# Performance work log

Measured on AMD Instinct MI355X. Metric: run time of the kernel, lower is better.

The kernel has to match this reference:

```python
import math
import jax, jax.numpy as jnp
import numpy as np

B, N, NR, DA, E, H, NB = 2, 2048, 256, 256, 768, 12, 2
DH = E // H
NQ, NK = 32, 128
INF = 1e10


def _layernorm(x, g=None, b=None, eps=1e-5):
    mu = x.mean(-1, keepdims=True)
    var = ((x - mu) ** 2).mean(-1, keepdims=True)
    y = (x - mu) * jax.lax.rsqrt(var + eps)
    if g is not None:
        y = y * g + b
    return y


def _fourier(x):
    # NeRF-style: freqs = 2**linspace(0,12,64); out dim = 3*(1+2*64) = 387
    freqs = 2.0 ** jnp.linspace(0.0, 12.0, 64)
    ang = (x[..., None, :] * freqs[:, None]).reshape(*x.shape[:-1], -1)  # (...,192)
    return jnp.concatenate([x, jnp.sin(ang), jnp.cos(ang)], -1)


def _abs_pos(pos):
    # sinusoidal absolute PE, embed_dim=DA//2, include_input -> DA//2 + 1 dims
    d = DA // 2
    div = jnp.exp(jnp.arange(0, d, 2, dtype=jnp.float32) * (-math.log(10000.0) / d))
    ang = pos * div  # (B,N,1)*(d/2,) -> (B,N,d/2)
    return jnp.concatenate([pos, jnp.sin(ang), jnp.cos(ang)], -1)


def _local_bias(n, nq, nk):
    # vectorized create_local_attn_bias: block-diagonal local window mask
    i = jnp.arange(n)
    blk = i // nq
    lo = jnp.maximum(0, nq * blk - (nk - nq) // 2)
    hi = nq * blk + (nq + nk) // 2
    j = jnp.arange(n)
    allowed = (j[None, :] >= lo[:, None]) & (j[None, :] < hi[:, None])
    return jnp.where(allowed, 0.0, -INF).astype(jnp.float32)


def _rope(x, pos):
    # x: (B,H,N,DH), pos: (B,N) float
    half = DH // 2
    inv = 1.0 / (10000.0 ** (jnp.arange(half, dtype=jnp.float32) / half))
    ang = pos[:, None, :, None] * inv  # (B,1,N,half)
    c, s = jnp.cos(ang), jnp.sin(ang)
    x1, x2 = x[..., :half], x[..., half:]
    return jnp.concatenate([x1 * c - x2 * s, x1 * s + x2 * c], -1)


def setup_inputs() -> dict:
    key = jax.random.key(0)
    def rn(i, shape, s=1.0):
        return jax.random.normal(jax.random.fold_in(key, i), shape, jnp.float32) * s
    LF = 387 + (DA // 2 + 1) + 408  # 924
    tok = (jnp.arange(N) * NR) // N  # each atom's residue index (sorted)
    inp = {
        'atom_coords': rn(0, (B, N, 3), 10.0),
        'ref_pos': rn(1, (B, N, 3), 10.0),
        'res_id': jnp.broadcast_to(tok[None, :, None], (B, N, 1)).astype(jnp.int32),
        'res_type_feat': rn(2, (B, N, 23)),
        'charge': rn(3, (B, N, 1)),
        'atomic_number': rn(4, (B, N, 128)),
        'atom_name_feat': rn(5, (B, N, 256)),
        'adaLN_emb': rn(6, (B, DA)),
        'rope_pos': jnp.broadcast_to(jnp.arange(N, dtype=jnp.int32)[None], (B, N)),
        'atom_to_token': jnp.broadcast_to(jax.nn.one_hot(tok, NR, dtype=jnp.float32)[None], (B, N, NR)),
        'feat_W': rn(7, (LF, DA), 0.02), 'feat_b': jnp.zeros(DA), 'feat_ln_g': jnp.ones(DA), 'feat_ln_b': jnp.zeros(DA),
        'pos_W': rn(8, (387, DA), 0.02),
        'in_W': rn(9, (2 * DA, DA), 0.02),
        'tin_W': rn(10, (DA, E), 0.02), 'tin_b': jnp.zeros(E), 'tin_ln_g': jnp.ones(E), 'tin_ln_b': jnp.zeros(E),
        'ada_W': rn(11, (DA, E), 0.02), 'ada_b': jnp.zeros(E), 'ada_ln_g': jnp.ones(E), 'ada_ln_b': jnp.zeros(E),
        'blk_mod_W': rn(12, (NB, E, 6 * E), 0.02), 'blk_mod_b': jnp.zeros((NB, 6 * E)),
        'blk_qkv_W': rn(13, (NB, E, 3 * E), 0.02), 'blk_qkv_b': jnp.zeros((NB, 3 * E)),
        'blk_o_W': rn(14, (NB, E, E), 0.02), 'blk_o_b': jnp.zeros((NB, E)),
        'blk_m1_W': rn(15, (NB, E, 4 * E), 0.02), 'blk_m1_b': jnp.zeros((NB, 4 * E)),
        'blk_m2_W': rn(16, (NB, 4 * E, E), 0.02), 'blk_m2_b': jnp.zeros((NB, E)),
        'tout_W': rn(17, (E, DA), 0.02), 'tout_b': jnp.zeros(DA), 'tout_ln_g': jnp.ones(DA), 'tout_ln_b': jnp.zeros(DA),
    }
    return inp


def reference(atom_coords, ref_pos, res_id, res_type_feat, charge, atomic_number,
              atom_name_feat, adaLN_emb, rope_pos, atom_to_token,
              feat_W, feat_b, feat_ln_g, feat_ln_b, pos_W, in_W,
              tin_W, tin_b, tin_ln_g, tin_ln_b, ada_W, ada_b, ada_ln_g, ada_ln_b,
              blk_mod_W, blk_mod_b, blk_qkv_W, blk_qkv_b, blk_o_W, blk_o_b,
              blk_m1_W, blk_m1_b, blk_m2_W, blk_m2_b,
              tout_W, tout_b, tout_ln_g, tout_ln_b):
    # feature fusion
    ref_pos_emb = _fourier(ref_pos)                                   # (B,N,387)
    atom_res_pos = _abs_pos(res_id.astype(jnp.float32))               # (B,N,129)
    feats = jnp.concatenate([ref_pos_emb, res_type_feat, atom_res_pos,
                             charge, atomic_number, atom_name_feat], -1)  # (B,N,924)
    feats = jax.nn.silu(_layernorm(feats @ feat_W + feat_b, feat_ln_g, feat_ln_b))
    coords = _fourier(atom_coords) @ pos_W                            # (B,N,DA)
    atom_in = jnp.concatenate([feats, coords], -1) @ in_W             # (B,N,DA)
    x = _layernorm(atom_in @ tin_W + tin_b, tin_ln_g, tin_ln_b)       # (B,N,E)
    c = _layernorm(adaLN_emb @ ada_W + ada_b, ada_ln_g, ada_ln_b)     # (B,E)

    bias = _local_bias(N, NQ, NK)                                     # (N,N)
    pos = rope_pos.astype(jnp.float32)
    scale = 1.0 / math.sqrt(DH)
    for l in range(NB):  # small fixed layer count
        m = jax.nn.silu(c) @ blk_mod_W[l] + blk_mod_b[l]
        sh1, sc1, g1, sh2, sc2, g2 = jnp.split(m, 6, -1)              # each (B,E)
        h = _layernorm(x) * (1 + sc1[:, None]) + sh1[:, None]
        qkv = (h @ blk_qkv_W[l] + blk_qkv_b[l]).reshape(B, N, 3, H, DH)
        q, k, v = [qkv[:, :, i].transpose(0, 2, 1, 3) for i in range(3)]  # (B,H,N,DH)
        q, k = _rope(q, pos), _rope(k, pos)
        scores = jnp.einsum('bhqd,bhkd->bhqk', q, k) * scale + bias
        attn = jax.nn.softmax(scores, -1)
        o = jnp.einsum('bhqk,bhkd->bhqd', attn, v).transpose(0, 2, 1, 3).reshape(B, N, E)
        x = x + g1[:, None] * (o @ blk_o_W[l] + blk_o_b[l])
        h2 = _layernorm(x) * (1 + sc2[:, None]) + sh2[:, None]
        x = x + g2[:, None] * (jax.nn.gelu(h2 @ blk_m1_W[l] + blk_m1_b[l]) @ blk_m2_W[l] + blk_m2_b[l])

    atom_latent = _layernorm(x @ tout_W + tout_b, tout_ln_g, tout_ln_b)   # (B,N,DA)
    a2t = atom_to_token / (atom_to_token.sum(1, keepdims=True) + 1e-6)    # segment-mean weights
    residue_latent = jnp.einsum('bnr,bnd->brd', a2t, atom_latent)         # (B,NR,DA)
    return residue_latent, atom_latent
```

## Files before the change

### kernel.cpp

```cpp
#include <hip/hip_runtime.h>
#include <hip/hip_bf16.h>
#include <math.h>

#define B_ 2
#define N_ 2048
#define NR_ 256
#define DA_ 256
#define E_ 768
#define H_ 12
#define DH_ 64
#define NB_ 2

typedef __attribute__((ext_vector_type(8))) __bf16 bf16x8;
typedef __attribute__((ext_vector_type(4))) float f32x4;

union U8 { bf16x8 v; __hip_bfloat16 e[8]; unsigned short u[8]; };
union U4 { __hip_bfloat16 e[4]; uint2 u2; };

__device__ __forceinline__ void gload16(const void* g, void* l) {
    __builtin_amdgcn_global_load_lds(
        (const __attribute__((address_space(1))) void*)g,
        (__attribute__((address_space(3))) void*)l, 16, 0, 0);
}

__device__ __forceinline__ float bsum256(float v, float* red4, int tid) {
    #pragma unroll
    for (int m = 32; m > 0; m >>= 1) v += __shfl_xor(v, m, 64);
    __syncthreads();
    if ((tid & 63) == 0) red4[tid >> 6] = v;
    __syncthreads();
    return red4[0] + red4[1] + red4[2] + red4[3];
}

__global__ __launch_bounds__(128) void build_feats_kernel(
    const float* __restrict__ atom_coords, const float* __restrict__ ref_pos,
    const int* __restrict__ res_id, const float* __restrict__ res_type,
    const float* __restrict__ charge, const float* __restrict__ atomic_number,
    const float* __restrict__ atom_name, const int* __restrict__ rope_pos,
    __hip_bfloat16* __restrict__ feats, __hip_bfloat16* __restrict__ coordsF,
    float* __restrict__ ropeC, float* __restrict__ ropeS)
{
    int a = blockIdx.x;
    int tid = threadIdx.x;
    __hip_bfloat16* f  = feats   + (size_t)a * 1024;
    __hip_bfloat16* cf = coordsF + (size_t)a * 512;

    float rp[3], cc[3];
    #pragma unroll
    for (int i = 0; i < 3; ++i) { rp[i] = ref_pos[(size_t)a*3 + i]; cc[i] = atom_coords[(size_t)a*3 + i]; }

    if (tid < 3) { f[tid] = __float2bfloat16(rp[tid]); cf[tid] = __float2bfloat16(cc[tid]); }

    if (tid >= 64 && tid < 96) {
        int dd = tid - 64;
        float rpos = (float)rope_pos[a];
        float ang = rpos * expf(-0.28782313662425574f * (float)dd);
        float sn, cs; sincosf(ang, &sn, &cs);
        ropeC[a*32 + dd] = cs; ropeS[a*32 + dd] = sn;
    }

    for (int s = tid; s < 192; s += 128) {
        int fi = s / 3, ci = s % 3;
        float freq = exp2f(12.f * (float)fi / 63.f);
        float ar = rp[ci] * freq;
        float ac = cc[ci] * freq;
        float snr, csr, snc, csc_;
        sincosf(ar, &snr, &csr);
        sincosf(ac, &snc, &csc_);
        f[3 + s]    = __float2bfloat16(snr);  f[195 + s]  = __float2bfloat16(csr);
        cf[3 + s]   = __float2bfloat16(snc);  cf[195 + s] = __float2bfloat16(csc_);
    }
    if (tid < 23) f[387 + tid] = __float2bfloat16(res_type[(size_t)a*23 + tid]);

    float pos = (float)res_id[a];
    if (tid == 0) f[410] = __float2bfloat16(pos);
    if (tid < 64) {
        float div = expf(-9.210340371976184f / 128.f * (float)(2 * tid));
        float ang = pos * div;
        float sn, cs; sincosf(ang, &sn, &cs);
        f[411 + tid] = __float2bfloat16(sn);
        f[475 + tid] = __float2bfloat16(cs);
    }
    if (tid == 0) f[539] = __float2bfloat16(charge[a]);
    if (tid < 128) f[540 + tid] = __float2bfloat16(atomic_number[(size_t)a*128 + tid]);
    for (int s = tid; s < 256; s += 128) f[668 + s] = __float2bfloat16(atom_name[(size_t)a*256 + s]);
    if (tid < 100) f[924 + tid] = __float2bfloat16(0.f);
    if (tid < 125) cf[387 + tid] = __float2bfloat16(0.f);
}

__global__ __launch_bounds__(256) void transconv_kernel(
    const float* __restrict__ W, __hip_bfloat16* __restrict__ WT,
    int Ksrc, int Kdst, int Nn, size_t wstride, size_t tstride)
{
    __shared__ float t[32][33];
    W  += (size_t)blockIdx.z * wstride;
    WT += (size_t)blockIdx.z * tstride;
    int n0 = blockIdx.x * 32, k0 = blockIdx.y * 32;
    int tid = threadIdx.x;
    int tx = tid & 31, ty = tid >> 5;
    #pragma unroll
    for (int i = 0; i < 4; ++i) {
        int k = k0 + ty + i*8;
        t[ty + i*8][tx] = (k < Ksrc) ? W[(size_t)k * Nn + n0 + tx] : 0.f;
    }
    __syncthreads();
    #pragma unroll
    for (int i = 0; i < 4; ++i) {
        int row = ty + i*8;
        WT[(size_t)(n0 + row) * Kdst + k0 + tx] = __float2bfloat16(t[tx][row]);
    }
}

__device__ __forceinline__ float epi_apply(float v, int grow, int gcol,
    const float* bias, int mode, const float* X, int ldx,
    const float* gate, int gstride)
{
    if (bias) v += bias[gcol];
    if (mode == 1) {
        float u = 1.5957691216057308f * (v + 0.044715f * v * v * v);
        v = v / (1.f + __expf(-u));
    } else if (mode == 2) {
        int b = grow >> 11;
        v = X[(size_t)grow * ldx + gcol] + gate[(size_t)b * gstride + gcol] * v;
    } else if (mode == 3) {
        v = v * gate[grow];
    }
    return v;
}

__global__ __launch_bounds__(256) void gemm_bf16_kernel(
    const __hip_bfloat16* __restrict__ A, int lda,
    const __hip_bfloat16* __restrict__ BT, int ldb,
    const float* __restrict__ bias,
    void* __restrict__ C, int ldc,
    int K, int mode, int obf,
    const float* __restrict__ X, int ldx,
    const float* __restrict__ gate, int gstride,
    float* __restrict__ P,
    int mtiles, size_t bstrideA, size_t bstrideB)
{
    __shared__ __hip_bfloat16 As[3][128 * 32];
    __shared__ __hip_bfloat16 Bs[3][128 * 32];

    int gx = gridDim.x;
    int nwg = gx * gridDim.y;
    int fo = blockIdx.y * gx + blockIdx.x;
    int ft = (fo & 7) * (nwg >> 3) + (fo >> 3);
    int bx = ft % gx, by = ft / gx;

    int bb  = by / mtiles;
    int m0l = (by % mtiles) * 128;
    int m0g = by * 128;
    int n0 = bx * 128;
    const __hip_bfloat16* Ab  = A  + (size_t)bb * bstrideA;
    const __hip_bfloat16* BTb = BT + (size_t)bb * bstrideB;
    int nz = gridDim.z;
    int Kh = K / nz;
    int kb = blockIdx.z * Kh;
    int nIter = Kh >> 5;
    int tid = threadIdx.x;
    int w = tid >> 6, l = tid & 63;
    int wr = (w >> 1) * 64, wc = (w & 1) * 64;
    int lr = l & 15, lg = l >> 4;
    int slot = ((lg ^ ((lr >> 1) & 3)) & 3) * 8;

    int seg0 = tid,        row0s = seg0 >> 2, g0 = (seg0 & 3) ^ ((row0s >> 1) & 3);
    int seg1 = 256 + tid,  row1s = seg1 >> 2, g1 = (seg1 & 3) ^ ((row1s >> 1) & 3);

    f32x4 acc[4][4];
    #pragma unroll
    for (int i = 0; i < 4; ++i)
        #pragma unroll
        for (int j = 0; j < 4; ++j)
            acc[i][j] = f32x4{0.f, 0.f, 0.f, 0.f};

    {
        gload16(Ab  + (size_t)(m0l + row0s) * lda + kb + g0 * 8, (char*)As[0] + seg0 * 16);
        gload16(BTb + (size_t)(n0 + row0s) * ldb + kb + g0 * 8, (char*)Bs[0] + seg0 * 16);
        gload16(Ab  + (size_t)(m0l + row1s) * lda + kb + g1 * 8, (char*)As[0] + seg1 * 16);
        gload16(BTb + (size_t)(n0 + row1s) * ldb + kb + g1 * 8, (char*)Bs[0] + seg1 * 16);
        if (nIter > 1) {
            int k1 = kb + 32;
            gload16(Ab  + (size_t)(m0l + row0s) * lda + k1 + g0 * 8, (char*)As[1] + seg0 * 16);
            gload16(BTb + (size_t)(n0 + row0s) * ldb + k1 + g0 * 8, (char*)Bs[1] + seg0 * 16);
            gload16(Ab  + (size_t)(m0l + row1s) * lda + k1 + g1 * 8, (char*)As[1] + seg1 * 16);
            gload16(BTb + (size_t)(n0 + row1s) * ldb + k1 + g1 * 8, (char*)Bs[1] + seg1 * 16);
        }
    }

    int cur = 0;
    for (int it = 0; it < nIter; ++it) {
        if (it + 1 < nIter) asm volatile("s_waitcnt vmcnt(4)" ::: "memory");
        else                asm volatile("s_waitcnt vmcnt(0)" ::: "memory");
        __builtin_amdgcn_s_barrier();
        __builtin_amdgcn_sched_barrier(0);
        if (it + 2 < nIter) {
            int nb = cur + 2; if (nb >= 3) nb -= 3;
            int kn = kb + (it + 2) * 32;
            gload16(Ab  + (size_t)(m0l + row0s) * lda + kn + g0 * 8, (char*)As[nb] + seg0 * 16);
            gload16(BTb + (size_t)(n0 + row0s) * ldb + kn + g0 * 8, (char*)Bs[nb] + seg0 * 16);
            gload16(Ab  + (size_t)(m0l + row1s) * lda + kn + g1 * 8, (char*)As[nb] + seg1 * 16);
            gload16(BTb + (size_t)(n0 + row1s) * ldb + kn + g1 * 8, (char*)Bs[nb] + seg1 * 16);
        }
        bf16x8 af[4], bfr[4];
        #pragma unroll
        for (int i = 0; i < 4; ++i) {
            af[i]  = *(bf16x8*)(As[cur] + (wr + i*16 + lr) * 32 + slot);
            bfr[i] = *(bf16x8*)(Bs[cur] + (wc + i*16 + lr) * 32 + slot);
        }
        #pragma unroll
        for (int i = 0; i < 4; ++i)
            #pragma unroll
            for (int j = 0; j < 4; ++j)
                acc[i][j] = __builtin_amdgcn_mfma_f32_16x16x32_bf16(af[i], bfr[j], acc[i][j], 0, 0, 0);
        cur = (cur == 2) ? 0 : cur + 1;
    }

    if (nz > 1) {
        int Nw = gridDim.x * 128;
        size_t pstride = (size_t)Nw * (gridDim.y * 128);
        float* Pz = P + (size_t)blockIdx.z * pstride;
        #pragma unroll
        for (int i = 0; i < 4; ++i)
            #pragma unroll
            for (int j = 0; j < 4; ++j)
                #pragma unroll
                for (int r = 0; r < 4; ++r) {
                    int grow = m0g + wr + i*16 + lg*4 + r;
                    int gcol = n0 + wc + j*16 + lr;
                    Pz[(size_t)grow * Nw + gcol] = acc[i][j][r];
                }
        return;
    }

    #pragma unroll
    for (int i = 0; i < 4; ++i)
        #pragma unroll
        for (int j = 0; j < 4; ++j)
            #pragma unroll
            for (int r = 0; r < 4; ++r) {
                int grow = m0g + wr + i*16 + lg*4 + r;
                int gcol = n0 + wc + j*16 + lr;
                float v = epi_apply(acc[i][j][r], grow, gcol, bias, mode, X, ldx, gate, gstride);
                if (obf)
                    ((__hip_bfloat16*)C)[(size_t)grow * ldc + gcol] = __float2bfloat16(v);
                else
                    ((float*)C)[(size_t)grow * ldc + gcol] = v;
            }
}

__global__ __launch_bounds__(256) void gcomb_kernel(
    const float* __restrict__ P, size_t pstride, int nz, int Nw,
    const float* __restrict__ bias,
    void* __restrict__ C, int ldc, int mode, int obf,
    const float* __restrict__ X, int ldx,
    const float* __restrict__ gate, int gstride,
    __hip_bfloat16* __restrict__ C2, int ldc2)
{
    int idx = blockIdx.x * 256 + threadIdx.x;
    int e0 = idx * 4;
    int grow = e0 / Nw, gc0 = e0 % Nw;
    float4 v = *(const float4*)(P + (size_t)grow * Nw + gc0);
    for (int z = 1; z < nz; ++z) {
        float4 t = *(const float4*)(P + (size_t)z * pstride + (size_t)grow * Nw + gc0);
        v.x += t.x; v.y += t.y; v.z += t.z; v.w += t.w;
    }
    float e[4] = {v.x, v.y, v.z, v.w};
    #pragma unroll
    for (int r = 0; r < 4; ++r)
        e[r] = epi_apply(e[r], grow, gc0 + r, bias, mode, X, ldx, gate, gstride);
    if (obf) {
        U4 o4;
        #pragma unroll
        for (int r = 0; r < 4; ++r) o4.e[r] = __float2bfloat16(e[r]);
        *(uint2*)((__hip_bfloat16*)C + (size_t)grow * ldc + gc0) = o4.u2;
    } else {
        *(float4*)((float*)C + (size_t)grow * ldc + gc0) = make_float4(e[0], e[1], e[2], e[3]);
    }
    if (C2) {
        U4 o4;
        #pragma unroll
        for (int r = 0; r < 4; ++r) o4.e[r] = __float2bfloat16(e[r]);
        *(uint2*)(C2 + (size_t)grow * ldc2 + gc0) = o4.u2;
    }
}

__global__ __launch_bounds__(256) void combln256_kernel(
    const float* __restrict__ P, size_t pstride, int nz,
    const float* __restrict__ bias,
    const float* __restrict__ g, const float* __restrict__ bv,
    int do_silu, int obf,
    void* __restrict__ out, int ldout)
{
    int row = blockIdx.x, d = threadIdx.x;
    __shared__ float red4[4];
    float v = P[(size_t)row*256 + d];
    for (int z = 1; z < nz; ++z) v += P[(size_t)z*pstride + (size_t)row*256 + d];
    v += bias[d];
    float mu = bsum256(v, red4, d) * (1.f/256.f);
    float dv = v - mu;
    float rstd = rsqrtf(bsum256(dv*dv, red4, d) * (1.f/256.f) + 1e-5f);
    float y = dv * rstd * g[d] + bv[d];
    if (do_silu) y = y / (1.f + __expf(-y));
    if (obf) ((__hip_bfloat16*)out)[(size_t)row * ldout + d] = __float2bfloat16(y);
    else     ((float*)out)[(size_t)row * ldout + d] = y;
}

__global__ __launch_bounds__(256) void tinfuse_kernel(
    const float* __restrict__ P, size_t pstride, int nz,
    const float* __restrict__ bias,
    const float* __restrict__ g, const float* __restrict__ bb,
    const float* __restrict__ scm, const float* __restrict__ shm,
    float* __restrict__ X, __hip_bfloat16* __restrict__ Hb)
{
    int row = blockIdx.x, tid = threadIdx.x;
    int b = row >> 11;
    __shared__ float red4[4];
    float tv[3];
    float s = 0.f;
    #pragma unroll
    for (int q = 0; q < 3; ++q) {
        int d = tid + q*256;
        float v = P[(size_t)row*768 + d];
        for (int z = 1; z < nz; ++z) v += P[(size_t)z*pstride + (size_t)row*768 + d];
        v += bias[d];
        tv[q] = v; s += v;
    }
    float mu1 = bsum256(s, red4, tid) * (1.f/768.f);
    float s2 = 0.f;
    #pragma unroll
    for (int q = 0; q < 3; ++q) { float dv = tv[q] - mu1; s2 += dv*dv; }
    float rstd1 = rsqrtf(bsum256(s2, red4, tid) * (1.f/768.f) + 1e-5f);
    float xv[3];
    float s3 = 0.f;
    #pragma unroll
    for (int q = 0; q < 3; ++q) {
        int d = tid + q*256;
        float y = (tv[q] - mu1) * rstd1 * g[d] + bb[d];
        X[(size_t)row*768 + d] = y;
        xv[q] = y; s3 += y;
    }
    float mu2 = bsum256(s3, red4, tid) * (1.f/768.f);
    float s4 = 0.f;
    #pragma unroll
    for (int q = 0; q < 3; ++q) { float dv = xv[q] - mu2; s4 += dv*dv; }
    float rstd2 = rsqrtf(bsum256(s4, red4, tid) * (1.f/768.f) + 1e-5f);
    #pragma unroll
    for (int q = 0; q < 3; ++q) {
        int d = tid + q*256;
        float h = (xv[q] - mu2) * rstd2 * (1.f + scm[(size_t)b*4608 + d]) + shm[(size_t)b*4608 + d];
        Hb[(size_t)row*768 + d] = __float2bfloat16(h);
    }
}

__global__ __launch_bounds__(256) void gcombln_kernel(
    const float* __restrict__ P, size_t pstride, int nz,
    const float* __restrict__ bias,
    float* __restrict__ X,
    const float* __restrict__ gate,
    const float* __restrict__ scm, const float* __restrict__ shm,
    __hip_bfloat16* __restrict__ Hb)
{
    int row = blockIdx.x, tid = threadIdx.x;
    int b = row >> 11;
    __shared__ float red4[4];
    float xv[3];
    float s = 0.f;
    #pragma unroll
    for (int q = 0; q < 3; ++q) {
        int d = tid + q*256;
        float v = P[(size_t)row*768 + d];
        for (int z = 1; z < nz; ++z) v += P[(size_t)z*pstride + (size_t)row*768 + d];
        v += bias[d];
        v = X[(size_t)row*768 + d] + gate[(size_t)b*4608 + d] * v;
        X[(size_t)row*768 + d] = v;
        xv[q] = v; s += v;
    }
    float mu = bsum256(s, red4, tid) * (1.f/768.f);
    float s2 = 0.f;
    #pragma unroll
    for (int q = 0; q < 3; ++q) { float dv = xv[q] - mu; s2 += dv*dv; }
    float rstd = rsqrtf(bsum256(s2, red4, tid) * (1.f/768.f) + 1e-5f);
    #pragma unroll
    for (int q = 0; q < 3; ++q) {
        int d = tid + q*256;
        float y = (xv[q] - mu) * rstd * (1.f + scm[(size_t)b*4608 + d]) + shm[(size_t)b*4608 + d];
        Hb[(size_t)row*768 + d] = __float2bfloat16(y);
    }
}

__global__ __launch_bounds__(256) void ada_kernel(
    const float* __restrict__ emb, const float* __restrict__ W,
    const float* __restrict__ bias,
    const float* __restrict__ g, const float* __restrict__ bb,
    float* __restrict__ c, float* __restrict__ c_silu)
{
    int b = blockIdx.x, tid = threadIdx.x;
    __shared__ float emb_s[256];
    __shared__ float t[768];
    __shared__ float red[256];
    emb_s[tid] = emb[b*256 + tid];
    __syncthreads();
    for (int q = 0; q < 3; ++q) {
        int e = tid + q*256;
        float acc = bias[e];
        for (int k = 0; k < 256; ++k) acc += emb_s[k] * W[(size_t)k*768 + e];
        t[e] = acc;
    }
    __syncthreads();
    float s = 0.f; for (int q = 0; q < 3; ++q) s += t[tid + q*256];
    red[tid] = s; __syncthreads();
    for (int off = 128; off > 0; off >>= 1) { if (tid < off) red[tid] += red[tid+off]; __syncthreads(); }
    float mu = red[0] / 768.f; __syncthreads();
    float s2 = 0.f; for (int q = 0; q < 3; ++q) { float d = t[tid + q*256] - mu; s2 += d*d; }
    red[tid] = s2; __syncthreads();
    for (int off = 128; off > 0; off >>= 1) { if (tid < off) red[tid] += red[tid+off]; __syncthreads(); }
    float rstd = rsqrtf(red[0] / 768.f + 1e-5f);
    for (int q = 0; q < 3; ++q) {
        int e = tid + q*256;
        float y = (t[e] - mu) * rstd * g[e] + bb[e];
        c[b*768 + e] = y;
        c_silu[b*768 + e] = y / (1.f + expf(-y));
    }
}

__global__ __launch_bounds__(256) void mod2_kernel(
    const float* __restrict__ c_silu, const float* __restrict__ mod_W,
    float* __restrict__ part)
{
    int idx = blockIdx.x * 256 + threadIdx.x;
    int z = blockIdx.y;
    int lyr = idx / 9216, b = (idx / 4608) & 1, j = idx % 4608;
    const float* Wl = mod_W + (size_t)lyr * 768 * 4608;
    const float* cs = c_silu + b * 768;
    float acc = 0.f;
    int k0 = z * 192;
    for (int k = k0; k < k0 + 192; ++k) acc += cs[k] * Wl[(size_t)k * 4608 + j];
    part[(size_t)z * 18432 + idx] = acc;
}

__global__ __launch_bounds__(256) void modc_kernel(
    const float* __restrict__ part, const float* __restrict__ mod_b,
    float* __restrict__ m2buf)
{
    int idx = blockIdx.x * 256 + threadIdx.x;
    int lyr = idx / 9216, j = idx % 4608;
    float acc = mod_b[(size_t)lyr * 4608 + j];
    #pragma unroll
    for (int z = 0; z < 4; ++z) acc += part[(size_t)z * 18432 + idx];
    m2buf[idx] = acc;
}

__global__ __launch_bounds__(64) void attn_mfma_kernel(
    const __hip_bfloat16* __restrict__ qkv,
    const float* __restrict__ ropeC,
    const float* __restrict__ ropeS,
    __hip_bfloat16* __restrict__ o)
{
    int bid = blockIdx.x;
    int qb = bid & 63;
    int h  = (bid >> 6) % 12;
    int b  = bid / 768;
    int l  = threadIdx.x;
    int lr = l & 15, lg = l >> 4;
    int lo = max(0, 32*qb - 48);
    int hi = min(N_, 32*qb + 80);
    int wlen = hi - lo;

    __shared__ __hip_bfloat16 Vl[128 * 72];
    __shared__ __hip_bfloat16 Pl[32 * 144];

    {
        int vr0 = l >> 3;
        int c0  = (l & 7) * 8;
        #pragma unroll
        for (int it = 0; it < 16; ++it) {
            int vr = it*8 + vr0;
            int n = lo + vr;
            U8 v;
            if (n < hi) {
                v.v = *(const bf16x8*)(qkv + ((size_t)(b*N_ + n))*2304 + 1536 + h*64 + c0);
            } else {
                #pragma unroll
                for (int j = 0; j < 8; ++j) v.u[j] = 0;
            }
            *(bf16x8*)(Vl + vr*72 + c0) = v.v;
        }
    }

    bf16x8 aq0[2], aq1[2];
    #pragma unroll
    for (int i = 0; i < 2; ++i) {
        int n = qb*32 + i*16 + lr;
        const __hip_bfloat16* qrow = qkv + ((size_t)(b*N_ + n))*2304 + h*64;
        U8 xlo, xhi;
        xlo.v = *(const bf16x8*)(qrow + lg*8);
        xhi.v = *(const bf16x8*)(qrow + 32 + lg*8);
        const float* pc = ropeC + ((size_t)(b*N_ + n))*32 + lg*8;
        const float* ps = ropeS + ((size_t)(b*N_ + n))*32 + lg*8;
        float4 c0 = *(const float4*)(pc), c1 = *(const float4*)(pc + 4);
        float4 s0 = *(const float4*)(ps), s1 = *(const float4*)(ps + 4);
        float cv[8] = {c0.x,c0.y,c0.z,c0.w,c1.x,c1.y,c1.z,c1.w};
        float sv[8] = {s0.x,s0.y,s0.z,s0.w,s1.x,s1.y,s1.z,s1.w};
        U8 f0, f1;
        #pragma unroll
        for (int j = 0; j < 8; ++j) {
            float x1 = __bfloat162float(xlo.e[j]);
            float x2 = __bfloat162float(xhi.e[j]);
            f0.e[j] = __float2bfloat16(x1*cv[j] - x2*sv[j]);
            f1.e[j] = __float2bfloat16(x1*sv[j] + x2*cv[j]);
        }
        aq0[i] = f0.v; aq1[i] = f1.v;
    }

    f32x4 S[2][8];
    #pragma unroll
    for (int i = 0; i < 2; ++i)
        #pragma unroll
        for (int jt = 0; jt < 8; ++jt)
            S[i][jt] = f32x4{0.f, 0.f, 0.f, 0.f};

    #pragma unroll
    for (int jt = 0; jt < 8; ++jt) {
        int n = lo + jt*16 + lr;
        U8 f0, f1;
        if (n < hi) {
            const __hip_bfloat16* krow = qkv + ((size_t)(b*N_ + n))*2304 + 768 + h*64;
            U8 xlo, xhi;
            xlo.v = *(const bf16x8*)(krow + lg*8);
            xhi.v = *(const bf16x8*)(krow + 32 + lg*8);
            const float* pc = ropeC + ((size_t)(b*N_ + n))*32 + lg*8;
            const float* ps = ropeS + ((size_t)(b*N_ + n))*32 + lg*8;
            float4 c0 = *(const float4*)(pc), c1 = *(const float4*)(pc + 4);
            float4 s0 = *(const float4*)(ps), s1 = *(const float4*)(ps + 4);
            float cv[8] = {c0.x,c0.y,c0.z,c0.w,c1.x,c1.y,c1.z,c1.w};
            float sv[8] = {s0.x,s0.y,s0.z,s0.w,s1.x,s1.y,s1.z,s1.w};
            #pragma unroll
            for (int j = 0; j < 8; ++j) {
                float x1 = __bfloat162float(xlo.e[j]);
                float x2 = __bfloat162float(xhi.e[j]);
                f0.e[j] = __float2bfloat16(x1*cv[j] - x2*sv[j]);
                f1.e[j] = __float2bfloat16(x1*sv[j] + x2*cv[j]);
            }
        } else {
            #pragma unroll
            for (int j = 0; j < 8; ++j) { f0.u[j] = 0; f1.u[j] = 0; }
        }
        #pragma unroll
        for (int i = 0; i < 2; ++i) {
            S[i][jt] = __builtin_amdgcn_mfma_f32_16x16x32_bf16(aq0[i], f0.v, S[i][jt], 0, 0, 0);
            S[i][jt] = __builtin_amdgcn_mfma_f32_16x16x32_bf16(aq1[i], f1.v, S[i][jt], 0, 0, 0);
        }
    }

    #pragma unroll
    for (int jt = 0; jt < 8; ++jt) {
        bool oob = (jt*16 + lr) >= wlen;
        #pragma unroll
        for (int i = 0; i < 2; ++i)
            #pragma unroll
            for (int r = 0; r < 4; ++r)
                S[i][jt][r] = oob ? -1e30f : S[i][jt][r] * 0.125f;
    }

    float rinv[2][4];
    #pragma unroll
    for (int i = 0; i < 2; ++i) {
        #pragma unroll
        for (int r = 0; r < 4; ++r) {
            float m = -1e30f;
            #pragma unroll
            for (int jt = 0; jt < 8; ++jt) m = fmaxf(m, S[i][jt][r]);
            #pragma unroll
            for (int mask = 8; mask > 0; mask >>= 1) m = fmaxf(m, __shfl_xor(m, mask, 16));
            float sum = 0.f;
            #pragma unroll
            for (int jt = 0; jt < 8; ++jt) {
                float e = __expf(S[i][jt][r] - m);
                S[i][jt][r] = e;
                sum += e;
            }
            #pragma unroll
            for (int mask = 8; mask > 0; mask >>= 1) sum += __shfl_xor(sum, mask, 16);
            rinv[i][r] = 1.f / sum;
        }
    }

    #pragma unroll
    for (int i = 0; i < 2; ++i)
        #pragma unroll
        for (int jt = 0; jt < 8; ++jt)
            #pragma unroll
            for (int r = 0; r < 4; ++r) {
                int row = i*16 + lg*4 + r;
                int colp = (jt*16 + lr) ^ (lg << 3);
                Pl[row*144 + colp] = __float2bfloat16(S[i][jt][r]);
            }

    __syncthreads();

    f32x4 O_[2][4];
    #pragma unroll
    for (int i = 0; i < 2; ++i)
        #pragma unroll
        for (int ct = 0; ct < 4; ++ct)
            O_[i][ct] = f32x4{0.f, 0.f, 0.f, 0.f};

    int key = (lr >> 2) & 3;
    #pragma unroll
    for (int kt = 0; kt < 4; ++kt) {
        bf16x8 pa[2];
        #pragma unroll
        for (int i = 0; i < 2; ++i) {
            int row = i*16 + lr;
            int colp = (kt*32 + lg*8) ^ (key << 3);
            pa[i] = *(bf16x8*)(Pl + row*144 + colp);
        }
        #pragma unroll
        for (int ct = 0; ct < 4; ++ct) {
            U8 bv;
            #pragma unroll
            for (int j = 0; j < 8; ++j)
                bv.e[j] = Vl[(kt*32 + lg*8 + j)*72 + ct*16 + lr];
            O_[0][ct] = __builtin_amdgcn_mfma_f32_16x16x32_bf16(pa[0], bv.v, O_[0][ct], 0, 0, 0);
            O_[1][ct] = __builtin_amdgcn_mfma_f32_16x16x32_bf16(pa[1], bv.v, O_[1][ct], 0, 0, 0);
        }
    }

    #pragma unroll
    for (int i = 0; i < 2; ++i)
        #pragma unroll
        for (int ct = 0; ct < 4; ++ct)
            #pragma unroll
            for (int r = 0; r < 4; ++r) {
                int row = qb*32 + i*16 + lg*4 + r;
                o[((size_t)(b*N_ + row))*768 + h*64 + ct*16 + lr] =
                    __float2bfloat16(O_[i][ct][r] * rinv[i][r]);
            }
}

__global__ __launch_bounds__(256) void a2t_transpose_kernel(
    const float* __restrict__ a2t, __hip_bfloat16* __restrict__ a2tTb)
{
    __shared__ float t[32][33];
    int r0 = blockIdx.x * 32, n0 = blockIdx.y * 32, b = blockIdx.z;
    int tid = threadIdx.x;
    int tx = tid & 31, ty = tid >> 5;
    #pragma unroll
    for (int i = 0; i < 4; ++i) {
        int row = ty + i*8;
        t[row][tx] = a2t[((size_t)b*N_ + n0 + row) * 256 + r0 + tx];
    }
    __syncthreads();
    #pragma unroll
    for (int i = 0; i < 4; ++i) {
        int row = ty + i*8;
        a2tTb[((size_t)b*256 + r0 + row) * N_ + n0 + tx] = __float2bfloat16(t[tx][row]);
    }
}

__global__ __launch_bounds__(256) void rowrecip_kernel(
    const __hip_bfloat16* __restrict__ a2tTb, float* __restrict__ recip)
{
    int row = blockIdx.x;
    int tid = threadIdx.x;
    __shared__ float red4[4];
    U8 v; v.v = *(const bf16x8*)(a2tTb + (size_t)row*2048 + tid*8);
    float s = 0.f;
    #pragma unroll
    for (int j = 0; j < 8; ++j) s += __bfloat162float(v.e[j]);
    float tot = bsum256(s, red4, tid);
    if (tid == 0) recip[row] = 1.f / (tot + 1e-6f);
}

extern "C" void kernel_launch(void* const* d_in, const int* in_sizes, int n_in,
                              void* d_out, int out_size, void* d_ws, size_t ws_size,
                              hipStream_t stream) {
    const float* atom_coords  = (const float*)d_in[0];
    const float* ref_pos      = (const float*)d_in[1];
    const int*   res_id       = (const int*)  d_in[2];
    const float* res_type     = (const float*)d_in[3];
    const float* charge       = (const float*)d_in[4];
    const float* atomic_num   = (const float*)d_in[5];
    const float* atom_name    = (const float*)d_in[6];
    const float* adaLN_emb    = (const float*)d_in[7];
    const int*   rope_pos     = (const int*)  d_in[8];
    const float* atom_to_tok  = (const float*)d_in[9];
    const float* feat_W       = (const float*)d_in[10];
    const float* feat_b       = (const float*)d_in[11];
    const float* feat_ln_g    = (const float*)d_in[12];
    const float* feat_ln_b    = (const float*)d_in[13];
    const float* pos_W        = (const float*)d_in[14];
    const float* in_W         = (const float*)d_in[15];
    const float* tin_W        = (const float*)d_in[16];
    const float* tin_b        = (const float*)d_in[17];
    const float* tin_ln_g     = (const float*)d_in[18];
    const float* tin_ln_b     = (const float*)d_in[19];
    const float* ada_W        = (const float*)d_in[20];
    const float* ada_b        = (const float*)d_in[21];
    const float* ada_ln_g     = (const float*)d_in[22];
    const float* ada_ln_b     = (const float*)d_in[23];
    const float* blk_mod_W    = (const float*)d_in[24];
    const float* blk_mod_b    = (const float*)d_in[25];
    const float* blk_qkv_W    = (const float*)d_in[26];
    const float* blk_qkv_b    = (const float*)d_in[27];
    const float* blk_o_W      = (const float*)d_in[28];
    const float* blk_o_b      = (const float*)d_in[29];
    const float* blk_m1_W     = (const float*)d_in[30];
    const float* blk_m1_b     = (const float*)d_in[31];
    const float* blk_m2_W     = (const float*)d_in[32];
    const float* blk_m2_b     = (const float*)d_in[33];
    const float* tout_W       = (const float*)d_in[34];
    const float* tout_b       = (const float*)d_in[35];
    const float* tout_ln_g    = (const float*)d_in[36];
    const float* tout_ln_b    = (const float*)d_in[37];

    const int BN = B_ * N_;
    float* ws = (float*)d_ws;

    const size_t OFF_X    = 0;
    const size_t OFF_HB   = OFF_X    + (size_t)BN*768;
    const size_t OFF_QKVB = OFF_HB   + (size_t)BN*768/2;
    const size_t OFF_OB   = OFF_QKVB + (size_t)BN*2304/2;
    const size_t OFF_UB   = OFF_OB   + (size_t)BN*768/2;
    const size_t OFF_WT   = OFF_UB   + (size_t)BN*3072/2;
    const size_t OFF_RC   = OFF_WT   + (size_t)3072*768/2;
    const size_t OFF_RS   = OFF_RC   + (size_t)BN*32;
    const size_t OFF_SM   = OFF_RS   + (size_t)BN*32;

    float* X = ws + OFF_X;
    __hip_bfloat16* Hb   = (__hip_bfloat16*)(ws + OFF_HB);
    __hip_bfloat16* QKVb = (__hip_bfloat16*)(ws + OFF_QKVB);
    __hip_bfloat16* Ob   = (__hip_bfloat16*)(ws + OFF_OB);
    __hip_bfloat16* Ub   = (__hip_bfloat16*)(ws + OFF_UB);
    __hip_bfloat16* WT   = (__hip_bfloat16*)(ws + OFF_WT);
    float* ropeC  = ws + OFF_RC;
    float* ropeS  = ws + OFF_RS;
    float* cbuf   = ws + OFF_SM;
    float* c_silu = cbuf + 1536;
    float* mbuf2  = c_silu + 1536;
    float* modpart= mbuf2 + 18432;

    __hip_bfloat16* featsB  = QKVb;
    __hip_bfloat16* coordsB = QKVb + (size_t)BN*1024;
    float* t1               = ws + OFF_UB;
    __hip_bfloat16* concatB = (__hip_bfloat16*)(t1 + (size_t)BN*256);
    __hip_bfloat16* atom_inB= Ob;

    __hip_bfloat16* a2tTb   = Ob;
    __hip_bfloat16* latTb   = Ob + (size_t)2*256*2048;
    float* recip            = modpart;

    float* P_pa   = ws + OFF_X;
    float* P_tin  = ws + OFF_UB;
    float* P_o    = ws + OFF_UB;
    float* P_m2   = ws + OFF_QKVB;
    float* P_tout = ws + OFF_UB;
    float* P_res  = ws + OFF_UB;

    float* out_res = (float*)d_out;
    float* out_lat = out_res + (size_t)B_*NR_*DA_;

    ada_kernel<<<2, 256, 0, stream>>>(adaLN_emb, ada_W, ada_b, ada_ln_g, ada_ln_b,
        cbuf, c_silu);
    mod2_kernel<<<dim3(72, 4), 256, 0, stream>>>(c_silu, blk_mod_W, modpart);
    modc_kernel<<<72, 256, 0, stream>>>(modpart, blk_mod_b, mbuf2);

    build_feats_kernel<<<BN, 128, 0, stream>>>(atom_coords, ref_pos, res_id,
        res_type, charge, atomic_num, atom_name, rope_pos, featsB, coordsB,
        ropeC, ropeS);

    transconv_kernel<<<dim3(8, 32), 256, 0, stream>>>(feat_W, WT, 924, 1024, 256, 0, 0);
    gemm_bf16_kernel<<<dim3(2, 32, 4), 256, 0, stream>>>(featsB, 1024, WT, 1024, nullptr,
        nullptr, 0, 1024, 0, 0, nullptr, 0, nullptr, 0, P_pa, 32, 0, 0);
    combln256_kernel<<<BN, 256, 0, stream>>>(P_pa, (size_t)BN*256, 4, feat_b,
        feat_ln_g, feat_ln_b, 1, 1, concatB, 512);
    transconv_kernel<<<dim3(8, 16), 256, 0, stream>>>(pos_W, WT, 387, 512, 256, 0, 0);
    gemm_bf16_kernel<<<dim3(2, 32, 4), 256, 0, stream>>>(coordsB, 512, WT, 512, nullptr,
        nullptr, 0, 512, 0, 0, nullptr, 0, nullptr, 0, P_pa, 32, 0, 0);
    gcomb_kernel<<<1024, 256, 0, stream>>>(P_pa, (size_t)BN*256, 4, 256, nullptr,
        concatB + 256, 512, 0, 1, nullptr, 0, nullptr, 0, nullptr, 0);
    transconv_kernel<<<dim3(8, 16), 256, 0, stream>>>(in_W, WT, 512, 512, 256, 0, 0);
    gemm_bf16_kernel<<<dim3(2, 32, 4), 256, 0, stream>>>(concatB, 512, WT, 512, nullptr,
        nullptr, 0, 512, 0, 0, nullptr, 0, nullptr, 0, P_pa, 32, 0, 0);
    gcomb_kernel<<<1024, 256, 0, stream>>>(P_pa, (size_t)BN*256, 4, 256, nullptr,
        atom_inB, 256, 0, 1, nullptr, 0, nullptr, 0, nullptr, 0);
    transconv_kernel<<<dim3(24, 8), 256, 0, stream>>>(tin_W, WT, 256, 256, 768, 0, 0);
    gemm_bf16_kernel<<<dim3(6, 32, 2), 256, 0, stream>>>(atom_inB, 256, WT, 256, nullptr,
        nullptr, 0, 256, 0, 0, nullptr, 0, nullptr, 0, P_tin, 32, 0, 0);
    tinfuse_kernel<<<BN, 256, 0, stream>>>(P_tin, (size_t)BN*768, 2, tin_b,
        tin_ln_g, tin_ln_b, mbuf2 + 768, mbuf2 + 0, X, Hb);

    for (int l = 0; l < NB_; ++l) {
        const float* qkvW = blk_qkv_W + (size_t)l*768*2304;
        const float* qkvB = blk_qkv_b + (size_t)l*2304;
        const float* oW   = blk_o_W   + (size_t)l*768*768;
        const float* oB   = blk_o_b   + (size_t)l*768;
        const float* m1W  = blk_m1_W  + (size_t)l*768*3072;
        const float* m1B  = blk_m1_b  + (size_t)l*3072;
        const float* m2W  = blk_m2_W  + (size_t)l*3072*768;
        const float* m2B  = blk_m2_b  + (size_t)l*768;

        float* mptr = mbuf2 + (size_t)l*9216;
        float* sh2 = mptr + 2304, *sc2 = mptr + 3072;
        float* g1  = mptr + 1536, *g2 = mptr + 3840;

        transconv_kernel<<<dim3(72, 24), 256, 0, stream>>>(qkvW, WT, 768, 768, 2304, 0, 0);
        gemm_bf16_kernel<<<dim3(18, 32, 1), 256, 0, stream>>>(Hb, 768, WT, 768, qkvB,
            QKVb, 2304, 768, 0, 1, nullptr, 0, nullptr, 0, nullptr, 32, 0, 0);
        attn_mfma_kernel<<<B_*H_*64, 64, 0, stream>>>(QKVb, ropeC, ropeS, Ob);
        transconv_kernel<<<dim3(24, 24), 256, 0, stream>>>(oW, WT, 768, 768, 768, 0, 0);
        gemm_bf16_kernel<<<dim3(6, 32, 2), 256, 0, stream>>>(Ob, 768, WT, 768, nullptr,
            nullptr, 0, 768, 0, 0, nullptr, 0, nullptr, 0, P_o, 32, 0, 0);
        gcombln_kernel<<<BN, 256, 0, stream>>>(P_o, (size_t)BN*768, 2, oB,
            X, g1, sc2, sh2, Hb);
        transconv_kernel<<<dim3(96, 24), 256, 0, stream>>>(m1W, WT, 768, 768, 3072, 0, 0);
        gemm_bf16_kernel<<<dim3(24, 32, 1), 256, 0, stream>>>(Hb, 768, WT, 768, m1B,
            Ub, 3072, 768, 1, 1, nullptr, 0, nullptr, 0, nullptr, 32, 0, 0);
        transconv_kernel<<<dim3(24, 96), 256, 0, stream>>>(m2W, WT, 3072, 3072, 768, 0, 0);
        gemm_bf16_kernel<<<dim3(6, 32, 2), 256, 0, stream>>>(Ub, 3072, WT, 3072, nullptr,
            nullptr, 0, 3072, 0, 0, nullptr, 0, nullptr, 0, P_m2, 32, 0, 0);
        if (l < NB_ - 1) {
            float* mnext = mbuf2 + (size_t)(l+1)*9216;
            gcombln_kernel<<<BN, 256, 0, stream>>>(P_m2, (size_t)BN*768, 2, m2B,
                X, g2, mnext + 768, mnext + 0, Hb);
        } else {
            gcomb_kernel<<<3072, 256, 0, stream>>>(P_m2, (size_t)BN*768, 2, 768, m2B,
                Hb, 768, 2, 1, X, 768, g2, 4608, nullptr, 0);
        }
    }

    transconv_kernel<<<dim3(8, 24), 256, 0, stream>>>(tout_W, WT, 768, 768, 256, 0, 0);
    gemm_bf16_kernel<<<dim3(2, 32, 4), 256, 0, stream>>>(Hb, 768, WT, 768, nullptr,
        nullptr, 0, 768, 0, 0, nullptr, 0, nullptr, 0, P_tout, 32, 0, 0);
    combln256_kernel<<<BN, 256, 0, stream>>>(P_tout, (size_t)BN*256, 4, tout_b,
        tout_ln_g, tout_ln_b, 0, 0, out_lat, 256);

    a2t_transpose_kernel<<<dim3(8, 64, 2), 256, 0, stream>>>(atom_to_tok, a2tTb);
    rowrecip_kernel<<<512, 256, 0, stream>>>(a2tTb, recip);
    transconv_kernel<<<dim3(8, 64, 2), 256, 0, stream>>>(out_lat, latTb, 2048, 2048, 256,
        (size_t)2048*256, (size_t)256*2048);
    gemm_bf16_kernel<<<dim3(2, 4, 8), 256, 0, stream>>>(a2tTb, 2048, latTb, 2048, nullptr,
        nullptr, 0, 2048, 0, 0, nullptr, 0, nullptr, 0, P_res,
        2, (size_t)256*2048, (size_t)256*2048);
    gcomb_kernel<<<128, 256, 0, stream>>>(P_res, (size_t)512*256, 8, 256, nullptr,
        out_res, 256, 3, 0, nullptr, 0, recip, 0, nullptr, 0);
}
```

Measured before the change: 590.7 us.

## Use 512-thread GEMM blocks with 8 waves and double buffering

```diff
diff --git a/kernel.cpp b/kernel.cpp
--- a/kernel.cpp
+++ b/kernel.cpp
@@ -128,7 +128,7 @@
     return v;
 }
 
-__global__ __launch_bounds__(256) void gemm_bf16_kernel(
+__global__ __launch_bounds__(512) void gemm_bf16_kernel(
     const __hip_bfloat16* __restrict__ A, int lda,
     const __hip_bfloat16* __restrict__ BT, int ldb,
     const float* __restrict__ bias,
@@ -139,8 +139,8 @@
     float* __restrict__ P,
     int mtiles, size_t bstrideA, size_t bstrideB)
 {
-    __shared__ __hip_bfloat16 As[3][128 * 32];
-    __shared__ __hip_bfloat16 Bs[3][128 * 32];
+    __shared__ __hip_bfloat16 As[2][128 * 32];
+    __shared__ __hip_bfloat16 Bs[2][128 * 32];
 
     int gx = gridDim.x;
     int nwg = gx * gridDim.y;
@@ -157,63 +157,48 @@
     int nz = gridDim.z;
     int Kh = K / nz;
     int kb = blockIdx.z * Kh;
-    int nIter = Kh >> 5;
     int tid = threadIdx.x;
     int w = tid >> 6, l = tid & 63;
-    int wr = (w >> 1) * 64, wc = (w & 1) * 64;
+    int wr = (w >> 2) * 64, wc = (w & 3) * 32;
     int lr = l & 15, lg = l >> 4;
     int slot = ((lg ^ ((lr >> 1) & 3)) & 3) * 8;
 
-    int seg0 = tid,        row0s = seg0 >> 2, g0 = (seg0 & 3) ^ ((row0s >> 1) & 3);
-    int seg1 = 256 + tid,  row1s = seg1 >> 2, g1 = (seg1 & 3) ^ ((row1s >> 1) & 3);
-
-    f32x4 acc[4][4];
+    int seg  = tid;
+    int rowS = seg >> 2;
+    int gS   = (seg & 3) ^ ((rowS >> 1) & 3);
+
+    f32x4 acc[4][2];
     #pragma unroll
     for (int i = 0; i < 4; ++i)
         #pragma unroll
-        for (int j = 0; j < 4; ++j)
+        for (int j = 0; j < 2; ++j)
             acc[i][j] = f32x4{0.f, 0.f, 0.f, 0.f};
 
-    {
-        gload16(Ab  + (size_t)(m0l + row0s) * lda + kb + g0 * 8, (char*)As[0] + seg0 * 16);
-        gload16(BTb + (size_t)(n0 + row0s) * ldb + kb + g0 * 8, (char*)Bs[0] + seg0 * 16);
-        gload16(Ab  + (size_t)(m0l + row1s) * lda + kb + g1 * 8, (char*)As[0] + seg1 * 16);
-        gload16(BTb + (size_t)(n0 + row1s) * ldb + kb + g1 * 8, (char*)Bs[0] + seg1 * 16);
-        if (nIter > 1) {
-            int k1 = kb + 32;
-            gload16(Ab  + (size_t)(m0l + row0s) * lda + k1 + g0 * 8, (char*)As[1] + seg0 * 16);
-            gload16(BTb + (size_t)(n0 + row0s) * ldb + k1 + g0 * 8, (char*)Bs[1] + seg0 * 16);
-            gload16(Ab  + (size_t)(m0l + row1s) * lda + k1 + g1 * 8, (char*)As[1] + seg1 * 16);
-            gload16(BTb + (size_t)(n0 + row1s) * ldb + k1 + g1 * 8, (char*)Bs[1] + seg1 * 16);
+    gload16(Ab  + (size_t)(m0l + rowS) * lda + kb + gS * 8, (char*)As[0] + seg * 16);
+    gload16(BTb + (size_t)(n0 + rowS) * ldb + kb + gS * 8, (char*)Bs[0] + seg * 16);
+
+    int cur = 0;
+    for (int k0 = kb; k0 < kb + Kh; k0 += 32) {
+        __syncthreads();
+        int kn = k0 + 32;
+        if (kn < kb + Kh) {
+            int nb = cur ^ 1;
+            gload16(Ab  + (size_t)(m0l + rowS) * lda + kn + gS * 8, (char*)As[nb] + seg * 16);
+            gload16(BTb + (size_t)(n0 + rowS) * ldb + kn + gS * 8, (char*)Bs[nb] + seg * 16);
         }
-    }
-
-    int cur = 0;
-    for (int it = 0; it < nIter; ++it) {
-        if (it + 1 < nIter) asm volatile("s_waitcnt vmcnt(4)" ::: "memory");
-        else                asm volatile("s_waitcnt vmcnt(0)" ::: "memory");
-        __builtin_amdgcn_s_barrier();
-        __builtin_amdgcn_sched_barrier(0);
-        if (it + 2 < nIter) {
-            int nb = cur + 2; if (nb >= 3) nb -= 3;
-            int kn = kb + (it + 2) * 32;
-            gload16(Ab  + (size_t)(m0l + row0s) * lda + kn + g0 * 8, (char*)As[nb] + seg0 * 16);
-            gload16(BTb + (size_t)(n0 + row0s) * ldb + kn + g0 * 8, (char*)Bs[nb] + seg0 * 16);
-            gload16(Ab  + (size_t)(m0l + row1s) * lda + kn + g1 * 8, (char*)As[nb] + seg1 * 16);
-            gload16(BTb + (size_t)(n0 + row1s) * ldb + kn + g1 * 8, (char*)Bs[nb] + seg1 * 16);
-        }
-        bf16x8 af[4], bfr[4];
-        #pragma unroll
-        for (int i = 0; i < 4; ++i) {
+        bf16x8 af[4], bfr[2];
+        #pragma unroll
+        for (int i = 0; i < 4; ++i)
             af[i]  = *(bf16x8*)(As[cur] + (wr + i*16 + lr) * 32 + slot);
-            bfr[i] = *(bf16x8*)(Bs[cur] + (wc + i*16 + lr) * 32 + slot);
-        }
+        #pragma unroll
+        for (int j = 0; j < 2; ++j)
+            bfr[j] = *(bf16x8*)(Bs[cur] + (wc + j*16 + lr) * 32 + slot);
         #pragma unroll
         for (int i = 0; i < 4; ++i)
             #pragma unroll
-            for (int j = 0; j < 4; ++j)
+            for (int j = 0; j < 2; ++j)
                 acc[i][j] = __builtin_amdgcn_mfma_f32_16x16x32_bf16(af[i], bfr[j], acc[i][j], 0, 0, 0);
-        cur = (cur == 2) ? 0 : cur + 1;
+        cur ^= 1;
     }
 
     if (nz > 1) {
@@ -223,7 +208,7 @@
         #pragma unroll
         for (int i = 0; i < 4; ++i)
             #pragma unroll
-            for (int j = 0; j < 4; ++j)
+            for (int j = 0; j < 2; ++j)
                 #pragma unroll
                 for (int r = 0; r < 4; ++r) {
                     int grow = m0g + wr + i*16 + lg*4 + r;
@@ -236,7 +221,7 @@
     #pragma unroll
     for (int i = 0; i < 4; ++i)
         #pragma unroll
-        for (int j = 0; j < 4; ++j)
+        for (int j = 0; j < 2; ++j)
             #pragma unroll
             for (int r = 0; r < 4; ++r) {
                 int grow = m0g + wr + i*16 + lg*4 + r;
@@ -771,22 +756,22 @@
         ropeC, ropeS);
 
     transconv_kernel<<<dim3(8, 32), 256, 0, stream>>>(feat_W, WT, 924, 1024, 256, 0, 0);
-    gemm_bf16_kernel<<<dim3(2, 32, 4), 256, 0, stream>>>(featsB, 1024, WT, 1024, nullptr,
+    gemm_bf16_kernel<<<dim3(2, 32, 4), 512, 0, stream>>>(featsB, 1024, WT, 1024, nullptr,
         nullptr, 0, 1024, 0, 0, nullptr, 0, nullptr, 0, P_pa, 32, 0, 0);
     combln256_kernel<<<BN, 256, 0, stream>>>(P_pa, (size_t)BN*256, 4, feat_b,
         feat_ln_g, feat_ln_b, 1, 1, concatB, 512);
     transconv_kernel<<<dim3(8, 16), 256, 0, stream>>>(pos_W, WT, 387, 512, 256, 0, 0);
-    gemm_bf16_kernel<<<dim3(2, 32, 4), 256, 0, stream>>>(coordsB, 512, WT, 512, nullptr,
+    gemm_bf16_kernel<<<dim3(2, 32, 4), 512, 0, stream>>>(coordsB, 512, WT, 512, nullptr,
         nullptr, 0, 512, 0, 0, nullptr, 0, nullptr, 0, P_pa, 32, 0, 0);
     gcomb_kernel<<<1024, 256, 0, stream>>>(P_pa, (size_t)BN*256, 4, 256, nullptr,
         concatB + 256, 512, 0, 1, nullptr, 0, nullptr, 0, nullptr, 0);
     transconv_kernel<<<dim3(8, 16), 256, 0, stream>>>(in_W, WT, 512, 512, 256, 0, 0);
-    gemm_bf16_kernel<<<dim3(2, 32, 4), 256, 0, stream>>>(concatB, 512, WT, 512, nullptr,
+    gemm_bf16_kernel<<<dim3(2, 32, 4), 512, 0, stream>>>(concatB, 512, WT, 512, nullptr,
         nullptr, 0, 512, 0, 0, nullptr, 0, nullptr, 0, P_pa, 32, 0, 0);
     gcomb_kernel<<<1024, 256, 0, stream>>>(P_pa, (size_t)BN*256, 4, 256, nullptr,
         atom_inB, 256, 0, 1, nullptr, 0, nullptr, 0, nullptr, 0);
     transconv_kernel<<<dim3(24, 8), 256, 0, stream>>>(tin_W, WT, 256, 256, 768, 0, 0);
-    gemm_bf16_kernel<<<dim3(6, 32, 2), 256, 0, stream>>>(atom_inB, 256, WT, 256, nullptr,
+    gemm_bf16_kernel<<<dim3(6, 32, 2), 512, 0, stream>>>(atom_inB, 256, WT, 256, nullptr,
         nullptr, 0, 256, 0, 0, nullptr, 0, nullptr, 0, P_tin, 32, 0, 0);
     tinfuse_kernel<<<BN, 256, 0, stream>>>(P_tin, (size_t)BN*768, 2, tin_b,
         tin_ln_g, tin_ln_b, mbuf2 + 768, mbuf2 + 0, X, Hb);
@@ -806,19 +791,19 @@
         float* g1  = mptr + 1536, *g2 = mptr + 3840;
 
         transconv_kernel<<<dim3(72, 24), 256, 0, stream>>>(qkvW, WT, 768, 768, 2304, 0, 0);
-        gemm_bf16_kernel<<<dim3(18, 32, 1), 256, 0, stream>>>(Hb, 768, WT, 768, qkvB,
+        gemm_bf16_kernel<<<dim3(18, 32, 1), 512, 0, stream>>>(Hb, 768, WT, 768, qkvB,
             QKVb, 2304, 768, 0, 1, nullptr, 0, nullptr, 0, nullptr, 32, 0, 0);
         attn_mfma_kernel<<<B_*H_*64, 64, 0, stream>>>(QKVb, ropeC, ropeS, Ob);
         transconv_kernel<<<dim3(24, 24), 256, 0, stream>>>(oW, WT, 768, 768, 768, 0, 0);
-        gemm_bf16_kernel<<<dim3(6, 32, 2), 256, 0, stream>>>(Ob, 768, WT, 768, nullptr,
+        gemm_bf16_kernel<<<dim3(6, 32, 2), 512, 0, stream>>>(Ob, 768, WT, 768, nullptr,
             nullptr, 0, 768, 0, 0, nullptr, 0, nullptr, 0, P_o, 32, 0, 0);
         gcombln_kernel<<<BN, 256, 0, stream>>>(P_o, (size_t)BN*768, 2, oB,
             X, g1, sc2, sh2, Hb);
         transconv_kernel<<<dim3(96, 24), 256, 0, stream>>>(m1W, WT, 768, 768, 3072, 0, 0);
-        gemm_bf16_kernel<<<dim3(24, 32, 1), 256, 0, stream>>>(Hb, 768, WT, 768, m1B,
+        gemm_bf16_kernel<<<dim3(24, 32, 1), 512, 0, stream>>>(Hb, 768, WT, 768, m1B,
             Ub, 3072, 768, 1, 1, nullptr, 0, nullptr, 0, nullptr, 32, 0, 0);
         transconv_kernel<<<dim3(24, 96), 256, 0, stream>>>(m2W, WT, 3072, 3072, 768, 0, 0);
-        gemm_bf16_kernel<<<dim3(6, 32, 2), 256, 0, stream>>>(Ub, 3072, WT, 3072, nullptr,
+        gemm_bf16_kernel<<<dim3(6, 32, 2), 512, 0, stream>>>(Ub, 3072, WT, 3072, nullptr,
             nullptr, 0, 3072, 0, 0, nullptr, 0, nullptr, 0, P_m2, 32, 0, 0);
         if (l < NB_ - 1) {
             float* mnext = mbuf2 + (size_t)(l+1)*9216;
@@ -831,7 +816,7 @@
     }
 
     transconv_kernel<<<dim3(8, 24), 256, 0, stream>>>(tout_W, WT, 768, 768, 256, 0, 0);
-    gemm_bf16_kernel<<<dim3(2, 32, 4), 256, 0, stream>>>(Hb, 768, WT, 768, nullptr,
+    gemm_bf16_kernel<<<dim3(2, 32, 4), 512, 0, stream>>>(Hb, 768, WT, 768, nullptr,
         nullptr, 0, 768, 0, 0, nullptr, 0, nullptr, 0, P_tout, 32, 0, 0);
     combln256_kernel<<<BN, 256, 0, stream>>>(P_tout, (size_t)BN*256, 4, tout_b,
         tout_ln_g, tout_ln_b, 0, 0, out_lat, 256);
@@ -840,7 +825,7 @@
     rowrecip_kernel<<<512, 256, 0, stream>>>(a2tTb, recip);
     transconv_kernel<<<dim3(8, 64, 2), 256, 0, stream>>>(out_lat, latTb, 2048, 2048, 256,
         (size_t)2048*256, (size_t)256*2048);
-    gemm_bf16_kernel<<<dim3(2, 4, 8), 256, 0, stream>>>(a2tTb, 2048, latTb, 2048, nullptr,
+    gemm_bf16_kernel<<<dim3(2, 4, 8), 512, 0, stream>>>(a2tTb, 2048, latTb, 2048, nullptr,
         nullptr, 0, 2048, 0, 0, nullptr, 0, nullptr, 0, P_res,
         2, (size_t)256*2048, (size_t)256*2048);
     gcomb_kernel<<<128, 256, 0, stream>>>(P_res, (size_t)512*256, 8, 256, nullptr,
```

After: 560.0 us. -5.2%, faster.
